# Performance work log

Measured on AMD Instinct MI355X. Metric: run time of the kernel, lower is better.

Reference implementation:

```python
import jax, jax.numpy as jnp
import numpy as np

N, E, DIM, HID, LAYERS = 100000, 600000, 128, 256, 2
LN_EPS = 1e-5


def setup_inputs() -> dict:
    key = jax.random.key(0)
    ks = jax.random.split(key, 16)
    h = jax.random.normal(ks[0], (N, DIM), dtype=jnp.float32)
    edge_index = jax.random.randint(ks[1], (E, 2), 0, N, dtype=jnp.int64)
    edge_attr = jax.random.uniform(ks[2], (E, 1), dtype=jnp.float32)
    s = 0.02
    # edge MLP: Linear(2*DIM+1, HID) -> GELU -> Linear(HID, 1) -> Sigmoid
    edge_w1 = jax.random.normal(ks[3], (LAYERS, 2 * DIM + 1, HID), dtype=jnp.float32) * s
    edge_b1 = jnp.zeros((LAYERS, HID), dtype=jnp.float32)
    edge_w2 = jax.random.normal(ks[4], (LAYERS, HID, 1), dtype=jnp.float32) * s
    edge_b2 = jnp.zeros((LAYERS, 1), dtype=jnp.float32)
    # node MLP: Linear(2*DIM, HID) -> GELU -> Linear(HID, DIM)
    node_w1 = jax.random.normal(ks[5], (LAYERS, 2 * DIM, HID), dtype=jnp.float32) * s
    node_b1 = jnp.zeros((LAYERS, HID), dtype=jnp.float32)
    node_w2 = jax.random.normal(ks[6], (LAYERS, HID, DIM), dtype=jnp.float32) * s
    node_b2 = jnp.zeros((LAYERS, DIM), dtype=jnp.float32)
    ln_g = jnp.ones((LAYERS, DIM), dtype=jnp.float32)
    ln_b = jnp.zeros((LAYERS, DIM), dtype=jnp.float32)
    return {"h": h, "edge_index": edge_index, "edge_attr": edge_attr,
            "edge_w1": edge_w1, "edge_b1": edge_b1, "edge_w2": edge_w2, "edge_b2": edge_b2,
            "node_w1": node_w1, "node_b1": node_b1, "node_w2": node_w2, "node_b2": node_b2,
            "ln_g": ln_g, "ln_b": ln_b}


def _layernorm(x, g, b):
    mu = jnp.mean(x, axis=-1, keepdims=True)
    var = jnp.mean(jnp.square(x - mu), axis=-1, keepdims=True)
    return (x - mu) * jax.lax.rsqrt(var + LN_EPS) * g + b


def reference(h, edge_index, edge_attr, edge_w1, edge_b1, edge_w2, edge_b2,
              node_w1, node_b1, node_w2, node_b2, ln_g, ln_b):
    src = edge_index[:, 0]
    dst = edge_index[:, 1]
    n = h.shape[0]
    for i in range(LAYERS):
        h_src = h[src]                                  # [E, DIM]
        h_dst = h[dst]                                  # [E, DIM]
        x = jnp.concatenate([h_src, h_dst, edge_attr], axis=-1)  # [E, 2*DIM+1]
        g1 = jax.nn.gelu(x @ edge_w1[i] + edge_b1[i], approximate=False)
        gate = jax.nn.sigmoid(g1 @ edge_w2[i] + edge_b2[i])       # [E, 1]
        msg = h_src * gate                              # [E, DIM]
        agg = jax.ops.segment_sum(msg, dst, num_segments=n)       # [N, DIM]
        den = jax.ops.segment_sum(gate, dst, num_segments=n)      # [N, 1]
        agg = agg / jnp.maximum(den, 1e-6)
        u = jnp.concatenate([h, agg], axis=-1)          # [N, 2*DIM]
        upd = jax.nn.gelu(u @ node_w1[i] + node_b1[i], approximate=False) @ node_w2[i] + node_b2[i]
        h = _layernorm(h + upd, ln_g[i], ln_b[i])
    return h
```

## Files before the change

### kernel.cpp

```cpp
#include <hip/hip_runtime.h>
#include <math.h>

#define NNODE 100000
#define NEDGE 600000
#define DIM 128
#define HID 256
#define NLAYERS 2

typedef short bf16x8 __attribute__((ext_vector_type(8)));
typedef short bf16x4 __attribute__((ext_vector_type(4)));
typedef float f32x4 __attribute__((ext_vector_type(4)));

#define WK 136
#define WLD 264

__device__ __forceinline__ short f2bf(float x) {
    union { float f; unsigned u; } v; v.f = x;
    unsigned r = v.u + 0x7FFFu + ((v.u >> 16) & 1u);
    return (short)(r >> 16);
}
__device__ __forceinline__ float bf2f(short s) {
    union { unsigned u; float f; } v; v.u = ((unsigned)(unsigned short)s) << 16;
    return v.f;
}
__device__ __forceinline__ float u_lo_f(unsigned u) {
    union { unsigned u; float f; } v; v.u = u << 16; return v.f;
}
__device__ __forceinline__ float u_hi_f(unsigned u) {
    union { unsigned u; float f; } v; v.u = u & 0xFFFF0000u; return v.f;
}
__device__ __forceinline__ float rf_f(float x) {
    return __int_as_float(__builtin_amdgcn_readfirstlane(__float_as_int(x)));
}
__device__ __forceinline__ float gelu_erf(float x) {
    float z = x * 0.70710678118654752f;
    float az = fabsf(z);
    float t = __builtin_amdgcn_rcpf(1.0f + 0.3275911f * az);
    float y = t * (0.254829592f + t * (-0.284496736f + t * (1.421413741f +
              t * (-1.453152027f + t * 1.061405429f))));
    float e = __expf(-az * az);
    float er = 1.0f - y * e;
    er = copysignf(er, z);
    return 0.5f * x * (1.0f + er);
}
__device__ __forceinline__ float gelu_fast(float x) {
    float e = exp2f(-2.4554673f * x);
    return x * __builtin_amdgcn_rcpf(1.0f + e);
}
__device__ __forceinline__ float sigmoid_fast(float z) {
    float e = exp2f(-1.4426950408889634f * z);
    return __builtin_amdgcn_rcpf(1.0f + e);
}

__global__ void prep_weights(const float* __restrict__ ew1,
                             const float* __restrict__ eb1,
                             const float* __restrict__ ew2,
                             const float* __restrict__ nw1,
                             const float* __restrict__ nw2,
                             const float* __restrict__ h0,
                             short* __restrict__ pW,
                             short* __restrict__ nW1T,
                             short* __restrict__ nW2T,
                             float* __restrict__ w1a_p,
                             float* __restrict__ b1_p,
                             float* __restrict__ w2_p,
                             short* __restrict__ hb)
{
    int idx = blockIdx.x * 256 + threadIdx.x;
    const int SZ1 = NLAYERS * 512 * 128;
    const int SZ2 = NLAYERS * 256 * 256;
    const int SZ3 = NLAYERS * 128 * 256;
    const int SZ4 = NLAYERS * 256;
    const int SZH = NNODE * DIM / 8;
    if (idx < SZ1) {
        int L = idx / (512 * 128); int rr = idx - L * 512 * 128;
        int r = rr >> 7, k = rr & 127;
        int srow = (r < 256) ? k : 128 + k;
        int scol = (r < 256) ? r : r - 256;
        pW[(size_t)L * 512 * WK + r * WK + k] = f2bf(ew1[(size_t)L * 257 * 256 + srow * 256 + scol]);
        return;
    }
    idx -= SZ1;
    if (idx < SZ2) {
        int L = idx >> 16, r = idx & 65535, n = r >> 8, k = r & 255;
        nW1T[(size_t)L * 256 * WLD + n * WLD + k] = f2bf(nw1[(size_t)L * 256 * 256 + k * 256 + n]);
        return;
    }
    idx -= SZ2;
    if (idx < SZ3) {
        int L = idx >> 15, r = idx & 32767, n = r >> 8, k = r & 255;
        nW2T[(size_t)L * 128 * WLD + n * WLD + k] = f2bf(nw2[(size_t)L * 256 * 128 + k * 128 + n]);
        return;
    }
    idx -= SZ3;
    if (idx < SZ4) {
        int L = idx >> 8, c = idx & 255;
        int cs = (c & ~63) | ((c & 3) * 16 + ((c >> 2) & 15));
        w1a_p[idx] = ew1[(size_t)L * 257 * 256 + 256 * 256 + cs];
        b1_p[idx]  = eb1[(size_t)L * 256 + cs];
        w2_p[idx]  = ew2[(size_t)L * 256 + cs];
        return;
    }
    idx -= SZ4;
    if (idx < SZH) {
        const float4* p = (const float4*)(h0 + (size_t)idx * 8);
        float4 a = p[0], b = p[1];
        bf16x8 t;
        t[0] = f2bf(a.x); t[1] = f2bf(a.y); t[2] = f2bf(a.z); t[3] = f2bf(a.w);
        t[4] = f2bf(b.x); t[5] = f2bf(b.y); t[6] = f2bf(b.z); t[7] = f2bf(b.w);
        *(bf16x8*)(hb + (size_t)idx * 8) = t;
    }
}

__global__ void csr_hist(const int* __restrict__ ei, int* __restrict__ deg) {
    int e = blockIdx.x * 256 + threadIdx.x;
    if (e >= NEDGE) return;
    atomicAdd(&deg[ei[2 * e + 1]], 1);
}

__global__ __launch_bounds__(1024)
void csr_scan(const int* __restrict__ deg, int* __restrict__ rowptr, int* __restrict__ cursor) {
    __shared__ int wsum[16];
    __shared__ int carry_s;
    const int tid = threadIdx.x, lane = tid & 63, wv = tid >> 6;
    if (tid == 0) carry_s = 0;
    __syncthreads();
    for (int base = 0; base < NNODE; base += 4096) {
        int i0 = base + tid * 4;
        int v0 = 0, v1 = 0, v2 = 0, v3 = 0;
        if (i0 + 3 < NNODE) {
            int4 q = *(const int4*)(deg + i0);
            v0 = q.x; v1 = q.y; v2 = q.z; v3 = q.w;
        } else if (i0 < NNODE) {
            v0 = deg[i0];
            if (i0 + 1 < NNODE) v1 = deg[i0 + 1];
            if (i0 + 2 < NNODE) v2 = deg[i0 + 2];
        }
        int tsum = v0 + v1 + v2 + v3;
        int x = tsum;
#pragma unroll
        for (int off = 1; off < 64; off <<= 1) {
            int y = __shfl_up(x, off);
            if (lane >= off) x += y;
        }
        if (lane == 63) wsum[wv] = x;
        __syncthreads();
        if (wv == 0) {
            int s = (lane < 16) ? wsum[lane] : 0;
#pragma unroll
            for (int off = 1; off < 16; off <<= 1) {
                int y = __shfl_up(s, off);
                if (lane >= off) s += y;
            }
            if (lane < 16) wsum[lane] = s;
        }
        __syncthreads();
        int carry = carry_s;
        int woff = wv ? wsum[wv - 1] : 0;
        int e0 = carry + woff + (x - tsum);
        if (i0 < NNODE)     { rowptr[i0] = e0;                cursor[i0] = e0; }
        if (i0 + 1 < NNODE) { int v = e0 + v0;                rowptr[i0+1] = v; cursor[i0+1] = v; }
        if (i0 + 2 < NNODE) { int v = e0 + v0 + v1;           rowptr[i0+2] = v; cursor[i0+2] = v; }
        if (i0 + 3 < NNODE) { int v = e0 + v0 + v1 + v2;      rowptr[i0+3] = v; cursor[i0+3] = v; }
        int total = wsum[15];
        __syncthreads();
        if (tid == 0) carry_s = carry + total;
        __syncthreads();
    }
    if (tid == 0) rowptr[NNODE] = carry_s;
}

__global__ void csr_scatter(const int* __restrict__ ei, const float* __restrict__ attr,
                            int* __restrict__ cursor,
                            int* __restrict__ esrc, float* __restrict__ attr_c) {
    int e = blockIdx.x * 256 + threadIdx.x;
    if (e >= NEDGE) return;
    int s = ei[2 * e], d = ei[2 * e + 1];
    int pos = atomicAdd(&cursor[d], 1);
    esrc[pos] = s;
    attr_c[pos] = attr[e];
}

__global__ __launch_bounds__(512, 2)
void proj_kernel(const short* __restrict__ hb,
                 const short* __restrict__ pW,
                 short* __restrict__ Ps,
                 short* __restrict__ Pd)
{
    __shared__ short A[64][WK];
    const int tid = threadIdx.x;
    const int n0 = blockIdx.x * 64;

    for (int idx = tid; idx < 64 * 16; idx += 512) {
        int nl = idx >> 4, q = idx & 15;
        int gn = min(n0 + nl, NNODE - 1);
        *(bf16x8*)&A[nl][q * 8] = *(const bf16x8*)(hb + (size_t)gn * DIM + q * 8);
    }
    __syncthreads();

    const int lane = tid & 63;
    const int wv = tid >> 6;
    const int lrow = lane & 15;
    const int lkg = lane >> 4;

    f32x4 acc[4][4];
#pragma unroll
    for (int mi = 0; mi < 4; ++mi)
#pragma unroll
        for (int ni = 0; ni < 4; ++ni) acc[mi][ni] = (f32x4){0.f, 0.f, 0.f, 0.f};

    const short* xbase = &A[lrow][lkg * 8];
    const short* wbase = pW + (size_t)(wv * 64 + lrow) * WK + lkg * 8;

#pragma unroll
    for (int kt = 0; kt < 4; ++kt) {
        bf16x8 a[4], b[4];
#pragma unroll
        for (int mi = 0; mi < 4; ++mi)
            a[mi] = *(const bf16x8*)(xbase + mi * 16 * WK + kt * 32);
#pragma unroll
        for (int ni = 0; ni < 4; ++ni)
            b[ni] = *(const bf16x8*)(wbase + ni * 16 * WK + kt * 32);
#pragma unroll
        for (int mi = 0; mi < 4; ++mi)
#pragma unroll
            for (int ni = 0; ni < 4; ++ni)
                acc[mi][ni] = __builtin_amdgcn_mfma_f32_16x16x32_bf16(a[mi], b[ni], acc[mi][ni], 0, 0, 0);
    }

    short* dstP = (wv < 4) ? Ps : Pd;
    const int cb = (wv & 3) * 64;
#pragma unroll
    for (int mi = 0; mi < 4; ++mi)
#pragma unroll
        for (int reg = 0; reg < 4; ++reg) {
            int node = n0 + mi * 16 + lkg * 4 + reg;
            bf16x4 t;
            t[0] = f2bf(acc[mi][0][reg]);
            t[1] = f2bf(acc[mi][1][reg]);
            t[2] = f2bf(acc[mi][2][reg]);
            t[3] = f2bf(acc[mi][3][reg]);
            if (node < NNODE)
                *(bf16x4*)(dstP + (size_t)node * 256 + cb + lrow * 4) = t;
        }
}

__global__ __launch_bounds__(256)
void edge_agg(const short* __restrict__ Ps, const short* __restrict__ Pd,
              const short* __restrict__ hb,
              const int* __restrict__ esrc, const int* __restrict__ rowptr,
              const float* __restrict__ attr_c,
              const float* __restrict__ w1a_p, const float* __restrict__ b1_p,
              const float* __restrict__ w2_p, const float* __restrict__ b2,
              short* __restrict__ u2)
{
    const int node = (blockIdx.x * 256 + threadIdx.x) >> 6;
    const int lane = threadIdx.x & 63;
    if (node >= NNODE) return;

    const int beg = __builtin_amdgcn_readfirstlane(rowptr[node]);
    const int end = __builtin_amdgcn_readfirstlane(rowptr[node + 1]);
    const int d = end - beg;

    const float4 w1av = ((const float4*)w1a_p)[lane];
    const float4 b1v  = ((const float4*)b1_p)[lane];
    const float4 w2v  = ((const float4*)w2_p)[lane];
    const float b2s = b2[0];

    bf16x4 pd = *(const bf16x4*)(Pd + (size_t)node * 256 + lane * 4);
    const float pb0 = bf2f(pd[0]) + b1v.x;
    const float pb1 = bf2f(pd[1]) + b1v.y;
    const float pb2 = bf2f(pd[2]) + b1v.z;
    const float pb3 = bf2f(pd[3]) + b1v.w;

    const int* ep = esrc + beg;
    const float* ap = attr_c + beg;
    const int pso = lane * 4;
    const int hvo = lane * 2;

    float ax = 0.f, ay = 0.f, den = 0.f;

    bf16x4 ps_n = (bf16x4){0, 0, 0, 0};
    unsigned hv_n = 0;
    float a_n = 0.f;
    if (d > 0) {
        int s0 = __builtin_amdgcn_readfirstlane(ep[0]);
        a_n = rf_f(ap[0]);
        ps_n = *(const bf16x4*)(Ps + ((size_t)s0 << 8) + pso);
        hv_n = *(const unsigned*)(hb + ((size_t)s0 << 7) + hvo);
    }
    for (int t = 0; t < d; ++t) {
        bf16x4 ps = ps_n; unsigned hv = hv_n; float a = a_n;
        if (t + 1 < d) {
            int s2 = __builtin_amdgcn_readfirstlane(ep[t + 1]);
            a_n = rf_f(ap[t + 1]);
            ps_n = *(const bf16x4*)(Ps + ((size_t)s2 << 8) + pso);
            hv_n = *(const unsigned*)(hb + ((size_t)s2 << 7) + hvo);
        }
        float x0 = bf2f(ps[0]) + pb0 + a * w1av.x;
        float x1 = bf2f(ps[1]) + pb1 + a * w1av.y;
        float x2 = bf2f(ps[2]) + pb2 + a * w1av.z;
        float x3 = bf2f(ps[3]) + pb3 + a * w1av.w;
        float p = gelu_fast(x0) * w2v.x + gelu_fast(x1) * w2v.y +
                  gelu_fast(x2) * w2v.z + gelu_fast(x3) * w2v.w;
        p += __shfl_xor(p, 1);
        p += __shfl_xor(p, 2);
        p += __shfl_xor(p, 4);
        p += __shfl_xor(p, 8);
        p += __shfl_xor(p, 16);
        p += __shfl_xor(p, 32);
        float g = sigmoid_fast(p + b2s);
        ax = fmaf(g, u_lo_f(hv), ax);
        ay = fmaf(g, u_hi_f(hv), ay);
        den += g;
    }

    float dd = fmaxf(den, 1e-6f);
    float dinv = __builtin_amdgcn_rcpf(dd);
    dinv = dinv * (2.0f - dd * dinv);
    unsigned pk = (((unsigned)(unsigned short)f2bf(ay * dinv)) << 16) |
                  (unsigned)(unsigned short)f2bf(ax * dinv);
    *(unsigned*)(u2 + (size_t)node * 256 + lane * 2) = pk;
}

__global__ __launch_bounds__(256, 4)
void node_mlp(const float* __restrict__ hin,
              const short* __restrict__ hb,
              const short* __restrict__ u2,
              const short* __restrict__ W1T,
              const float* __restrict__ b1,
              const short* __restrict__ W2T,
              const float* __restrict__ b2,
              const float* __restrict__ lng, const float* __restrict__ lnb,
              float* __restrict__ hout, short* __restrict__ hb_out)
{
    __shared__ short U[32][WLD];
    __shared__ short G[32][WLD];

    const int tid = threadIdx.x;
    const int n0 = blockIdx.x * 32;
    const int lane = tid & 63;
    const int wv = tid >> 6;

    for (int idx = tid; idx < 32 * 32; idx += 256) {
        int nl = idx >> 5, q = idx & 31;
        const short* src = (q < 16) ? (hb + (size_t)(n0 + nl) * DIM + q * 8)
                                    : (u2 + (size_t)(n0 + nl) * 256 + (q - 16) * 8);
        *(bf16x8*)&U[nl][q * 8] = *(const bf16x8*)src;
    }
    __syncthreads();

    const int lrow = lane & 15;
    const int lkg = lane >> 4;

    {
        const int n0w = wv * 64;
        f32x4 acc1[2][4];
#pragma unroll
        for (int mi = 0; mi < 2; ++mi)
#pragma unroll
            for (int ni = 0; ni < 4; ++ni) acc1[mi][ni] = (f32x4){0.f, 0.f, 0.f, 0.f};

        const short* xbase = &U[lrow][lkg * 8];
        const short* wbase = W1T + (size_t)(n0w + lrow) * WLD + lkg * 8;
#pragma unroll
        for (int kt = 0; kt < 8; ++kt) {
            bf16x8 a[2], b[4];
#pragma unroll
            for (int mi = 0; mi < 2; ++mi)
                a[mi] = *(const bf16x8*)(xbase + mi * 16 * WLD + kt * 32);
#pragma unroll
            for (int ni = 0; ni < 4; ++ni)
                b[ni] = *(const bf16x8*)(wbase + ni * 16 * WLD + kt * 32);
#pragma unroll
            for (int mi = 0; mi < 2; ++mi)
#pragma unroll
                for (int ni = 0; ni < 4; ++ni)
                    acc1[mi][ni] = __builtin_amdgcn_mfma_f32_16x16x32_bf16(a[mi], b[ni], acc1[mi][ni], 0, 0, 0);
        }

        float b1v[4];
#pragma unroll
        for (int ni = 0; ni < 4; ++ni) b1v[ni] = b1[n0w + ni * 16 + lrow];
#pragma unroll
        for (int mi = 0; mi < 2; ++mi)
#pragma unroll
            for (int ni = 0; ni < 4; ++ni)
#pragma unroll
                for (int reg = 0; reg < 4; ++reg) {
                    int row = mi * 16 + lkg * 4 + reg;
                    int col = n0w + ni * 16 + lrow;
                    G[row][col] = f2bf(gelu_erf(acc1[mi][ni][reg] + b1v[ni]));
                }
    }
    __syncthreads();

    float* R = (float*)&U[0][0];
    {
        f32x4 acc2[2][2];
#pragma unroll
        for (int mi = 0; mi < 2; ++mi)
#pragma unroll
            for (int ni = 0; ni < 2; ++ni) acc2[mi][ni] = (f32x4){0.f, 0.f, 0.f, 0.f};

        const short* xbase = &G[lrow][lkg * 8];
        const short* wbase = W2T + (size_t)(wv * 32 + lrow) * WLD + lkg * 8;
#pragma unroll
        for (int kt = 0; kt < 8; ++kt) {
            bf16x8 a[2], b[2];
#pragma unroll
            for (int mi = 0; mi < 2; ++mi)
                a[mi] = *(const bf16x8*)(xbase + mi * 16 * WLD + kt * 32);
#pragma unroll
            for (int ni = 0; ni < 2; ++ni)
                b[ni] = *(const bf16x8*)(wbase + ni * 16 * WLD + kt * 32);
#pragma unroll
            for (int mi = 0; mi < 2; ++mi)
#pragma unroll
                for (int ni = 0; ni < 2; ++ni)
                    acc2[mi][ni] = __builtin_amdgcn_mfma_f32_16x16x32_bf16(a[mi], b[ni], acc2[mi][ni], 0, 0, 0);
        }

        float b2v[2];
#pragma unroll
        for (int ni = 0; ni < 2; ++ni) b2v[ni] = b2[wv * 32 + ni * 16 + lrow];
#pragma unroll
        for (int mi = 0; mi < 2; ++mi)
#pragma unroll
            for (int ni = 0; ni < 2; ++ni)
#pragma unroll
                for (int reg = 0; reg < 4; ++reg) {
                    int row = mi * 16 + lkg * 4 + reg;
                    int col = wv * 32 + ni * 16 + lrow;
                    R[row * 132 + col] = acc2[mi][ni][reg] + b2v[ni];
                }
    }
    __syncthreads();

#pragma unroll
    for (int ii = 0; ii < 8; ++ii) {
        int nl = wv * 8 + ii;
        int gn = n0 + nl;
        float rx = R[nl * 132 + lane * 2 + 0];
        float ry = R[nl * 132 + lane * 2 + 1];
        const float2 hh = *(const float2*)(hin + (size_t)gn * DIM + lane * 2);
        float vx = rx + hh.x, vy = ry + hh.y;
        float s = vx + vy;
#pragma unroll
        for (int off = 32; off > 0; off >>= 1) s += __shfl_xor(s, off);
        float mu = s * (1.0f / 128.0f);
        float dx = vx - mu, dy = vy - mu;
        float q = dx * dx + dy * dy;
#pragma unroll
        for (int off = 32; off > 0; off >>= 1) q += __shfl_xor(q, off);
        float inv = rsqrtf(q * (1.0f / 128.0f) + 1e-5f);
        const float2 gg = *(const float2*)(lng + lane * 2);
        const float2 bb = *(const float2*)(lnb + lane * 2);
        float ox = dx * inv * gg.x + bb.x;
        float oy = dy * inv * gg.y + bb.y;
        *(float2*)(hout + (size_t)gn * DIM + lane * 2) = make_float2(ox, oy);
        unsigned pk = ((unsigned)(unsigned short)f2bf(oy) << 16) |
                      (unsigned)(unsigned short)f2bf(ox);
        *(unsigned*)(hb_out + (size_t)gn * DIM + lane * 2) = pk;
    }
}

extern "C" void kernel_launch(void* const* d_in, const int* in_sizes, int n_in,
                              void* d_out, int out_size, void* d_ws, size_t ws_size,
                              hipStream_t stream) {
    const float* h0   = (const float*)d_in[0];
    const int*   ei   = (const int*)d_in[1];
    const float* attr = (const float*)d_in[2];
    const float* ew1  = (const float*)d_in[3];
    const float* eb1  = (const float*)d_in[4];
    const float* ew2  = (const float*)d_in[5];
    const float* eb2  = (const float*)d_in[6];
    const float* nw1  = (const float*)d_in[7];
    const float* nb1  = (const float*)d_in[8];
    const float* nw2  = (const float*)d_in[9];
    const float* nb2  = (const float*)d_in[10];
    const float* lng  = (const float*)d_in[11];
    const float* lnb  = (const float*)d_in[12];

    float* hout = (float*)d_out;

    char* p = (char*)d_ws;
    int*   rowptr = (int*)p;               p += sizeof(int) * (NNODE + 4);
    int*   cursor = (int*)p;               p += sizeof(int) * (NNODE + 4);
    int*   deg    = (int*)p;               p += sizeof(int) * (NNODE + 4);
    int*   esrc   = (int*)p;               p += sizeof(int) * NEDGE;
    float* attr_c = (float*)p;             p += sizeof(float) * NEDGE;
    short* hb     = (short*)p;             p += sizeof(short) * (size_t)NNODE * DIM;
    short* Ps     = (short*)p;             p += sizeof(short) * (size_t)NNODE * 256;
    short* Pd     = (short*)p;             p += sizeof(short) * (size_t)NNODE * 256;
    short* u2     = Pd;
    short* pW     = (short*)p;             p += sizeof(short) * (size_t)NLAYERS * 512 * WK;
    short* nW1T   = (short*)p;             p += sizeof(short) * (size_t)NLAYERS * 256 * WLD;
    short* nW2T   = (short*)p;             p += sizeof(short) * (size_t)NLAYERS * 128 * WLD;
    float* w1a_p  = (float*)p;             p += sizeof(float) * NLAYERS * 256;
    float* b1_p   = (float*)p;             p += sizeof(float) * NLAYERS * 256;
    float* w2_p   = (float*)p;             p += sizeof(float) * NLAYERS * 256;

    const int PREP_TOTAL = NLAYERS * 512 * 128 + NLAYERS * 256 * 256 +
                           NLAYERS * 128 * 256 + NLAYERS * 256 + NNODE * DIM / 8;

    hipMemsetAsync(deg, 0, (NNODE + 1) * sizeof(int), stream);
    prep_weights<<<(PREP_TOTAL + 255) / 256, 256, 0, stream>>>(
        ew1, eb1, ew2, nw1, nw2, h0, pW, nW1T, nW2T, w1a_p, b1_p, w2_p, hb);
    csr_hist<<<(NEDGE + 255) / 256, 256, 0, stream>>>(ei, deg);
    csr_scan<<<1, 1024, 0, stream>>>(deg, rowptr, cursor);
    csr_scatter<<<(NEDGE + 255) / 256, 256, 0, stream>>>(ei, attr, cursor, esrc, attr_c);

    for (int L = 0; L < NLAYERS; ++L) {
        const float* hin = (L == 0) ? h0 : hout;
        proj_kernel<<<(NNODE + 63) / 64, 512, 0, stream>>>(
            hb, pW + (size_t)L * 512 * WK, Ps, Pd);
        edge_agg<<<(NNODE + 3) / 4, 256, 0, stream>>>(
            Ps, Pd, hb, esrc, rowptr, attr_c,
            w1a_p + (size_t)L * 256, b1_p + (size_t)L * 256,
            w2_p + (size_t)L * 256, eb2 + L, u2);
        node_mlp<<<NNODE / 32, 256, 0, stream>>>(
            hin, hb, u2,
            nW1T + (size_t)L * 256 * WLD, nb1 + (size_t)L * 256,
            nW2T + (size_t)L * 128 * WLD, nb2 + (size_t)L * 128,
            lng + (size_t)L * DIM, lnb + (size_t)L * DIM,
            hout, hb);
    }
}
```

Measured before the change: 521.0 us.

## Fuse degree histogram into prep, pack edge arrays, rework edge_agg math, enlarge node_mlp tile

The degree histogram moves into the prep_weights launch, removing one kernel launch. Source indices and edge attributes are packed into a single int2 array, so each edge needs one load instead of two. A sentinel entry makes the prefetch in the edge loop unconditional. The edge GELU-sigmoid path is rewritten with paired float2 math and one shared reciprocal per pair of activations. node_mlp processes 64 nodes per block instead of 32, which doubles shared memory and registers per block and lowers the occupancy hint from 4 to 2, in exchange for more weight reuse per block.

After: 602.0 us. 15.5% more time.

```diff
diff --git a/kernel.cpp b/kernel.cpp
--- a/kernel.cpp
+++ b/kernel.cpp
@@ -10,6 +10,8 @@
 typedef short bf16x8 __attribute__((ext_vector_type(8)));
 typedef short bf16x4 __attribute__((ext_vector_type(4)));
 typedef float f32x4 __attribute__((ext_vector_type(4)));
+typedef float f32x2 __attribute__((ext_vector_type(2)));
+typedef unsigned u32x2 __attribute__((ext_vector_type(2)));
 
 #define WK 136
 #define WLD 264
@@ -23,14 +25,11 @@
     union { unsigned u; float f; } v; v.u = ((unsigned)(unsigned short)s) << 16;
     return v.f;
 }
-__device__ __forceinline__ float u_lo_f(unsigned u) {
+__device__ __forceinline__ float bits_lo(unsigned u) {
     union { unsigned u; float f; } v; v.u = u << 16; return v.f;
 }
-__device__ __forceinline__ float u_hi_f(unsigned u) {
+__device__ __forceinline__ float bits_hi(unsigned u) {
     union { unsigned u; float f; } v; v.u = u & 0xFFFF0000u; return v.f;
-}
-__device__ __forceinline__ float rf_f(float x) {
-    return __int_as_float(__builtin_amdgcn_readfirstlane(__float_as_int(x)));
 }
 __device__ __forceinline__ float gelu_erf(float x) {
     float z = x * 0.70710678118654752f;
@@ -43,10 +42,6 @@
     er = copysignf(er, z);
     return 0.5f * x * (1.0f + er);
 }
-__device__ __forceinline__ float gelu_fast(float x) {
-    float e = exp2f(-2.4554673f * x);
-    return x * __builtin_amdgcn_rcpf(1.0f + e);
-}
 __device__ __forceinline__ float sigmoid_fast(float z) {
     float e = exp2f(-1.4426950408889634f * z);
     return __builtin_amdgcn_rcpf(1.0f + e);
@@ -58,13 +53,15 @@
                              const float* __restrict__ nw1,
                              const float* __restrict__ nw2,
                              const float* __restrict__ h0,
+                             const int* __restrict__ ei,
                              short* __restrict__ pW,
                              short* __restrict__ nW1T,
                              short* __restrict__ nW2T,
                              float* __restrict__ w1a_p,
                              float* __restrict__ b1_p,
                              float* __restrict__ w2_p,
-                             short* __restrict__ hb)
+                             short* __restrict__ hb,
+                             int* __restrict__ deg)
 {
     int idx = blockIdx.x * 256 + threadIdx.x;
     const int SZ1 = NLAYERS * 512 * 128;
@@ -109,13 +106,12 @@
         t[0] = f2bf(a.x); t[1] = f2bf(a.y); t[2] = f2bf(a.z); t[3] = f2bf(a.w);
         t[4] = f2bf(b.x); t[5] = f2bf(b.y); t[6] = f2bf(b.z); t[7] = f2bf(b.w);
         *(bf16x8*)(hb + (size_t)idx * 8) = t;
-    }
-}
-
-__global__ void csr_hist(const int* __restrict__ ei, int* __restrict__ deg) {
-    int e = blockIdx.x * 256 + threadIdx.x;
-    if (e >= NEDGE) return;
-    atomicAdd(&deg[ei[2 * e + 1]], 1);
+        return;
+    }
+    idx -= SZH;
+    if (idx < NEDGE) {
+        atomicAdd(&deg[ei[2 * idx + 1]], 1);
+    }
 }
 
 __global__ __launch_bounds__(1024)
@@ -171,14 +167,14 @@
 }
 
 __global__ void csr_scatter(const int* __restrict__ ei, const float* __restrict__ attr,
-                            int* __restrict__ cursor,
-                            int* __restrict__ esrc, float* __restrict__ attr_c) {
+                            int* __restrict__ cursor, int2* __restrict__ epk) {
     int e = blockIdx.x * 256 + threadIdx.x;
     if (e >= NEDGE) return;
     int s = ei[2 * e], d = ei[2 * e + 1];
     int pos = atomicAdd(&cursor[d], 1);
-    esrc[pos] = s;
-    attr_c[pos] = attr[e];
+    int2 pk; pk.x = s; pk.y = __float_as_int(attr[e]);
+    epk[pos] = pk;
+    if (e == 0) { int2 z; z.x = 0; z.y = 0; epk[NEDGE] = z; }
 }
 
 __global__ __launch_bounds__(512, 2)
@@ -248,8 +244,7 @@
 __global__ __launch_bounds__(256)
 void edge_agg(const short* __restrict__ Ps, const short* __restrict__ Pd,
               const short* __restrict__ hb,
-              const int* __restrict__ esrc, const int* __restrict__ rowptr,
-              const float* __restrict__ attr_c,
+              const int2* __restrict__ epk, const int* __restrict__ rowptr,
               const float* __restrict__ w1a_p, const float* __restrict__ b1_p,
               const float* __restrict__ w2_p, const float* __restrict__ b2,
               short* __restrict__ u2)
@@ -266,43 +261,58 @@
     const float4 b1v  = ((const float4*)b1_p)[lane];
     const float4 w2v  = ((const float4*)w2_p)[lane];
     const float b2s = b2[0];
+    const f32x2 w1a01 = {w1av.x, w1av.y}, w1a23 = {w1av.z, w1av.w};
+    const f32x2 w2_01 = {w2v.x, w2v.y},  w2_23 = {w2v.z, w2v.w};
 
     bf16x4 pd = *(const bf16x4*)(Pd + (size_t)node * 256 + lane * 4);
-    const float pb0 = bf2f(pd[0]) + b1v.x;
-    const float pb1 = bf2f(pd[1]) + b1v.y;
-    const float pb2 = bf2f(pd[2]) + b1v.z;
-    const float pb3 = bf2f(pd[3]) + b1v.w;
-
-    const int* ep = esrc + beg;
-    const float* ap = attr_c + beg;
+    const f32x2 pb01 = {bf2f(pd[0]) + b1v.x, bf2f(pd[1]) + b1v.y};
+    const f32x2 pb23 = {bf2f(pd[2]) + b1v.z, bf2f(pd[3]) + b1v.w};
+
+    const int2* ep = epk + beg;
     const int pso = lane * 4;
     const int hvo = lane * 2;
 
-    float ax = 0.f, ay = 0.f, den = 0.f;
-
-    bf16x4 ps_n = (bf16x4){0, 0, 0, 0};
+    f32x2 axy = {0.f, 0.f};
+    float den = 0.f;
+
+    u32x2 ps_n = (u32x2){0, 0};
     unsigned hv_n = 0;
     float a_n = 0.f;
     if (d > 0) {
-        int s0 = __builtin_amdgcn_readfirstlane(ep[0]);
-        a_n = rf_f(ap[0]);
-        ps_n = *(const bf16x4*)(Ps + ((size_t)s0 << 8) + pso);
+        int2 sa = ep[0];
+        int s0 = __builtin_amdgcn_readfirstlane(sa.x);
+        a_n = __int_as_float(__builtin_amdgcn_readfirstlane(sa.y));
+        ps_n = *(const u32x2*)(Ps + ((size_t)s0 << 8) + pso);
         hv_n = *(const unsigned*)(hb + ((size_t)s0 << 7) + hvo);
     }
+    const float KNEG = -2.4554673f;
     for (int t = 0; t < d; ++t) {
-        bf16x4 ps = ps_n; unsigned hv = hv_n; float a = a_n;
-        if (t + 1 < d) {
-            int s2 = __builtin_amdgcn_readfirstlane(ep[t + 1]);
-            a_n = rf_f(ap[t + 1]);
-            ps_n = *(const bf16x4*)(Ps + ((size_t)s2 << 8) + pso);
+        u32x2 psu = ps_n; unsigned hv = hv_n; float a = a_n;
+        {
+            int2 sa = ep[t + 1];
+            int s2 = __builtin_amdgcn_readfirstlane(sa.x);
+            a_n = __int_as_float(__builtin_amdgcn_readfirstlane(sa.y));
+            ps_n = *(const u32x2*)(Ps + ((size_t)s2 << 8) + pso);
             hv_n = *(const unsigned*)(hb + ((size_t)s2 << 7) + hvo);
         }
-        float x0 = bf2f(ps[0]) + pb0 + a * w1av.x;
-        float x1 = bf2f(ps[1]) + pb1 + a * w1av.y;
-        float x2 = bf2f(ps[2]) + pb2 + a * w1av.z;
-        float x3 = bf2f(ps[3]) + pb3 + a * w1av.w;
-        float p = gelu_fast(x0) * w2v.x + gelu_fast(x1) * w2v.y +
-                  gelu_fast(x2) * w2v.z + gelu_fast(x3) * w2v.w;
+        f32x2 ps01, ps23;
+        ps01[0] = bits_lo(psu[0]); ps01[1] = bits_hi(psu[0]);
+        ps23[0] = bits_lo(psu[1]); ps23[1] = bits_hi(psu[1]);
+        const f32x2 av = {a, a};
+        f32x2 x01 = av * w1a01 + (ps01 + pb01);
+        f32x2 x23 = av * w1a23 + (ps23 + pb23);
+        f32x2 m01 = x01 * KNEG;
+        f32x2 m23 = x23 * KNEG;
+        float A0 = 1.f + exp2f(m01[0]);
+        float A1 = 1.f + exp2f(m01[1]);
+        float A2 = 1.f + exp2f(m23[0]);
+        float A3 = 1.f + exp2f(m23[1]);
+        f32x2 t01 = x01 * w2_01;
+        f32x2 t23 = x23 * w2_23;
+        float num01 = t01[0] * A1 + t01[1] * A0;
+        float num23 = t23[0] * A3 + t23[1] * A2;
+        float p = num01 * __builtin_amdgcn_rcpf(A0 * A1)
+                + num23 * __builtin_amdgcn_rcpf(A2 * A3);
         p += __shfl_xor(p, 1);
         p += __shfl_xor(p, 2);
         p += __shfl_xor(p, 4);
@@ -310,20 +320,22 @@
         p += __shfl_xor(p, 16);
         p += __shfl_xor(p, 32);
         float g = sigmoid_fast(p + b2s);
-        ax = fmaf(g, u_lo_f(hv), ax);
-        ay = fmaf(g, u_hi_f(hv), ay);
+        f32x2 hxy;
+        hxy[0] = bits_lo(hv); hxy[1] = bits_hi(hv);
+        const f32x2 gv = {g, g};
+        axy = gv * hxy + axy;
         den += g;
     }
 
     float dd = fmaxf(den, 1e-6f);
     float dinv = __builtin_amdgcn_rcpf(dd);
     dinv = dinv * (2.0f - dd * dinv);
-    unsigned pk = (((unsigned)(unsigned short)f2bf(ay * dinv)) << 16) |
-                  (unsigned)(unsigned short)f2bf(ax * dinv);
+    unsigned pk = (((unsigned)(unsigned short)f2bf(axy[1] * dinv)) << 16) |
+                  (unsigned)(unsigned short)f2bf(axy[0] * dinv);
     *(unsigned*)(u2 + (size_t)node * 256 + lane * 2) = pk;
 }
 
-__global__ __launch_bounds__(256, 4)
+__global__ __launch_bounds__(256, 2)
 void node_mlp(const float* __restrict__ hin,
               const short* __restrict__ hb,
               const short* __restrict__ u2,
@@ -334,18 +346,19 @@
               const float* __restrict__ lng, const float* __restrict__ lnb,
               float* __restrict__ hout, short* __restrict__ hb_out)
 {
-    __shared__ short U[32][WLD];
-    __shared__ short G[32][WLD];
+    __shared__ short U[64][WLD];
+    __shared__ short G[64][WLD];
 
     const int tid = threadIdx.x;
-    const int n0 = blockIdx.x * 32;
+    const int n0 = blockIdx.x * 64;
     const int lane = tid & 63;
     const int wv = tid >> 6;
 
-    for (int idx = tid; idx < 32 * 32; idx += 256) {
+    for (int idx = tid; idx < 64 * 32; idx += 256) {
         int nl = idx >> 5, q = idx & 31;
-        const short* src = (q < 16) ? (hb + (size_t)(n0 + nl) * DIM + q * 8)
-                                    : (u2 + (size_t)(n0 + nl) * 256 + (q - 16) * 8);
+        int gn = min(n0 + nl, NNODE - 1);
+        const short* src = (q < 16) ? (hb + (size_t)gn * DIM + q * 8)
+                                    : (u2 + (size_t)gn * 256 + (q - 16) * 8);
         *(bf16x8*)&U[nl][q * 8] = *(const bf16x8*)src;
     }
     __syncthreads();
@@ -355,9 +368,9 @@
 
     {
         const int n0w = wv * 64;
-        f32x4 acc1[2][4];
-#pragma unroll
-        for (int mi = 0; mi < 2; ++mi)
+        f32x4 acc1[4][4];
+#pragma unroll
+        for (int mi = 0; mi < 4; ++mi)
 #pragma unroll
             for (int ni = 0; ni < 4; ++ni) acc1[mi][ni] = (f32x4){0.f, 0.f, 0.f, 0.f};
 
@@ -365,15 +378,15 @@
         const short* wbase = W1T + (size_t)(n0w + lrow) * WLD + lkg * 8;
 #pragma unroll
         for (int kt = 0; kt < 8; ++kt) {
-            bf16x8 a[2], b[4];
-#pragma unroll
-            for (int mi = 0; mi < 2; ++mi)
+            bf16x8 a[4], b[4];
+#pragma unroll
+            for (int mi = 0; mi < 4; ++mi)
                 a[mi] = *(const bf16x8*)(xbase + mi * 16 * WLD + kt * 32);
 #pragma unroll
             for (int ni = 0; ni < 4; ++ni)
                 b[ni] = *(const bf16x8*)(wbase + ni * 16 * WLD + kt * 32);
 #pragma unroll
-            for (int mi = 0; mi < 2; ++mi)
+            for (int mi = 0; mi < 4; ++mi)
 #pragma unroll
                 for (int ni = 0; ni < 4; ++ni)
                     acc1[mi][ni] = __builtin_amdgcn_mfma_f32_16x16x32_bf16(a[mi], b[ni], acc1[mi][ni], 0, 0, 0);
@@ -383,7 +396,7 @@
 #pragma unroll
         for (int ni = 0; ni < 4; ++ni) b1v[ni] = b1[n0w + ni * 16 + lrow];
 #pragma unroll
-        for (int mi = 0; mi < 2; ++mi)
+        for (int mi = 0; mi < 4; ++mi)
 #pragma unroll
             for (int ni = 0; ni < 4; ++ni)
 #pragma unroll
@@ -397,9 +410,9 @@
 
     float* R = (float*)&U[0][0];
     {
-        f32x4 acc2[2][2];
-#pragma unroll
-        for (int mi = 0; mi < 2; ++mi)
+        f32x4 acc2[4][2];
+#pragma unroll
+        for (int mi = 0; mi < 4; ++mi)
 #pragma unroll
             for (int ni = 0; ni < 2; ++ni) acc2[mi][ni] = (f32x4){0.f, 0.f, 0.f, 0.f};
 
@@ -407,15 +420,15 @@
         const short* wbase = W2T + (size_t)(wv * 32 + lrow) * WLD + lkg * 8;
 #pragma unroll
         for (int kt = 0; kt < 8; ++kt) {
-            bf16x8 a[2], b[2];
-#pragma unroll
-            for (int mi = 0; mi < 2; ++mi)
+            bf16x8 a[4], b[2];
+#pragma unroll
+            for (int mi = 0; mi < 4; ++mi)
                 a[mi] = *(const bf16x8*)(xbase + mi * 16 * WLD + kt * 32);
 #pragma unroll
             for (int ni = 0; ni < 2; ++ni)
                 b[ni] = *(const bf16x8*)(wbase + ni * 16 * WLD + kt * 32);
 #pragma unroll
-            for (int mi = 0; mi < 2; ++mi)
+            for (int mi = 0; mi < 4; ++mi)
 #pragma unroll
                 for (int ni = 0; ni < 2; ++ni)
                     acc2[mi][ni] = __builtin_amdgcn_mfma_f32_16x16x32_bf16(a[mi], b[ni], acc2[mi][ni], 0, 0, 0);
@@ -425,7 +438,7 @@
 #pragma unroll
         for (int ni = 0; ni < 2; ++ni) b2v[ni] = b2[wv * 32 + ni * 16 + lrow];
 #pragma unroll
-        for (int mi = 0; mi < 2; ++mi)
+        for (int mi = 0; mi < 4; ++mi)
 #pragma unroll
             for (int ni = 0; ni < 2; ++ni)
 #pragma unroll
@@ -438,12 +451,13 @@
     __syncthreads();
 
 #pragma unroll
-    for (int ii = 0; ii < 8; ++ii) {
-        int nl = wv * 8 + ii;
+    for (int ii = 0; ii < 16; ++ii) {
+        int nl = wv * 16 + ii;
         int gn = n0 + nl;
+        int gnc = min(gn, NNODE - 1);
         float rx = R[nl * 132 + lane * 2 + 0];
         float ry = R[nl * 132 + lane * 2 + 1];
-        const float2 hh = *(const float2*)(hin + (size_t)gn * DIM + lane * 2);
+        const float2 hh = *(const float2*)(hin + (size_t)gnc * DIM + lane * 2);
         float vx = rx + hh.x, vy = ry + hh.y;
         float s = vx + vy;
 #pragma unroll
@@ -454,14 +468,16 @@
 #pragma unroll
         for (int off = 32; off > 0; off >>= 1) q += __shfl_xor(q, off);
         float inv = rsqrtf(q * (1.0f / 128.0f) + 1e-5f);
-        const float2 gg = *(const float2*)(lng + lane * 2);
-        const float2 bb = *(const float2*)(lnb + lane * 2);
-        float ox = dx * inv * gg.x + bb.x;
-        float oy = dy * inv * gg.y + bb.y;
-        *(float2*)(hout + (size_t)gn * DIM + lane * 2) = make_float2(ox, oy);
-        unsigned pk = ((unsigned)(unsigned short)f2bf(oy) << 16) |
-                      (unsigned)(unsigned short)f2bf(ox);
-        *(unsigned*)(hb_out + (size_t)gn * DIM + lane * 2) = pk;
+        if (gn < NNODE) {
+            const float2 gg = *(const float2*)(lng + lane * 2);
+            const float2 bb = *(const float2*)(lnb + lane * 2);
+            float ox = dx * inv * gg.x + bb.x;
+            float oy = dy * inv * gg.y + bb.y;
+            *(float2*)(hout + (size_t)gn * DIM + lane * 2) = make_float2(ox, oy);
+            unsigned pk = ((unsigned)(unsigned short)f2bf(oy) << 16) |
+                          (unsigned)(unsigned short)f2bf(ox);
+            *(unsigned*)(hb_out + (size_t)gn * DIM + lane * 2) = pk;
+        }
     }
 }
 
@@ -488,8 +504,7 @@
     int*   rowptr = (int*)p;               p += sizeof(int) * (NNODE + 4);
     int*   cursor = (int*)p;               p += sizeof(int) * (NNODE + 4);
     int*   deg    = (int*)p;               p += sizeof(int) * (NNODE + 4);
-    int*   esrc   = (int*)p;               p += sizeof(int) * NEDGE;
-    float* attr_c = (float*)p;             p += sizeof(float) * NEDGE;
+    int2*  epk    = (int2*)p;              p += sizeof(int2) * (NEDGE + 1);
     short* hb     = (short*)p;             p += sizeof(short) * (size_t)NNODE * DIM;
     short* Ps     = (short*)p;             p += sizeof(short) * (size_t)NNODE * 256;
     short* Pd     = (short*)p;             p += sizeof(short) * (size_t)NNODE * 256;
@@ -502,24 +517,23 @@
     float* w2_p   = (float*)p;             p += sizeof(float) * NLAYERS * 256;
 
     const int PREP_TOTAL = NLAYERS * 512 * 128 + NLAYERS * 256 * 256 +
-                           NLAYERS * 128 * 256 + NLAYERS * 256 + NNODE * DIM / 8;
+                           NLAYERS * 128 * 256 + NLAYERS * 256 + NNODE * DIM / 8 + NEDGE;
 
     hipMemsetAsync(deg, 0, (NNODE + 1) * sizeof(int), stream);
     prep_weights<<<(PREP_TOTAL + 255) / 256, 256, 0, stream>>>(
-        ew1, eb1, ew2, nw1, nw2, h0, pW, nW1T, nW2T, w1a_p, b1_p, w2_p, hb);
-    csr_hist<<<(NEDGE + 255) / 256, 256, 0, stream>>>(ei, deg);
+        ew1, eb1, ew2, nw1, nw2, h0, ei, pW, nW1T, nW2T, w1a_p, b1_p, w2_p, hb, deg);
     csr_scan<<<1, 1024, 0, stream>>>(deg, rowptr, cursor);
-    csr_scatter<<<(NEDGE + 255) / 256, 256, 0, stream>>>(ei, attr, cursor, esrc, attr_c);
+    csr_scatter<<<(NEDGE + 255) / 256, 256, 0, stream>>>(ei, attr, cursor, epk);
 
     for (int L = 0; L < NLAYERS; ++L) {
         const float* hin = (L == 0) ? h0 : hout;
         proj_kernel<<<(NNODE + 63) / 64, 512, 0, stream>>>(
             hb, pW + (size_t)L * 512 * WK, Ps, Pd);
         edge_agg<<<(NNODE + 3) / 4, 256, 0, stream>>>(
-            Ps, Pd, hb, esrc, rowptr, attr_c,
+            Ps, Pd, hb, epk, rowptr,
             w1a_p + (size_t)L * 256, b1_p + (size_t)L * 256,
             w2_p + (size_t)L * 256, eb2 + L, u2);
-        node_mlp<<<NNODE / 32, 256, 0, stream>>>(
+        node_mlp<<<(NNODE + 63) / 64, 256, 0, stream>>>(
             hin, hb, u2,
             nW1T + (size_t)L * 256 * WLD, nb1 + (size_t)L * 256,
             nW2T + (size_t)L * 128 * WLD, nb2 + (size_t)L * 128,
```
